# Optimization experiments

Measured on AMD Instinct MI355X. Metric: run time of the kernel, lower is better.

Reference implementation:

```python
import jax, jax.numpy as jnp
import numpy as np
import math

N_HEADS = 16
D_MODEL = 1024
D_K = D_MODEL // N_HEADS
B, T = 16, 512


def setup_inputs() -> dict:
    key = jax.random.key(0)
    ks = jax.random.split(key, 8)
    x = jax.random.normal(ks[0], (B, T, D_MODEL), dtype=jnp.float32)
    mask = jnp.ones((B, 1, T), dtype=bool)
    pos = jax.random.normal(ks[1], (1, 2 * T - 1, D_MODEL), dtype=jnp.float32)
    s = 1.0 / math.sqrt(D_MODEL)
    qvk_w = jax.random.normal(ks[2], (D_MODEL, 3 * D_MODEL), dtype=jnp.float32) * s
    qvk_b = jnp.zeros((3 * D_MODEL,), dtype=jnp.float32)
    pos_w = jax.random.normal(ks[3], (D_MODEL, D_MODEL), dtype=jnp.float32) * s
    # xavier_normal on [1,1,nh,d_k]
    pstd = math.sqrt(2.0 / (N_HEADS + D_K))
    posu = jax.random.normal(ks[4], (1, 1, N_HEADS, D_K), dtype=jnp.float32) * pstd
    posv = jax.random.normal(ks[5], (1, 1, N_HEADS, D_K), dtype=jnp.float32) * pstd
    return {"x": x, "mask": mask, "pos": pos, "qvk_w": qvk_w, "qvk_b": qvk_b,
            "pos_w": pos_w, "posu": posu, "posv": posv}


def _shift(matrix_bd):
    # matrix_bd: [b, nh, t, 2t-1] -> gather relative positions -> [b, nh, t, t]
    b, nh, t, _ = matrix_bd.shape
    r = jnp.arange(t)
    rel_pos = (r[None, :] - r[:, None]) + (t - 1)          # [t, t]
    idx = rel_pos[None, None]                               # [1,1,t,t]
    return jnp.take_along_axis(matrix_bd, jnp.broadcast_to(idx, (b, nh, t, t)), axis=3)


def reference(x, mask, pos, qvk_w, qvk_b, pos_w, posu, posv):
    b, t, d = x.shape
    nh, dk = N_HEADS, D_K
    h = x @ qvk_w + qvk_b                                   # [b, t, 3d]
    q, k, v = jnp.split(h, 3, axis=-1)
    q = q.reshape(b, t, nh, dk)                             # [b, t, nh, dk]
    k = k.reshape(b, t, nh, dk).transpose(0, 2, 1, 3)       # [b, nh, t, dk]
    v = v.reshape(b, t, nh, dk).transpose(0, 2, 1, 3)
    p = (pos @ pos_w).reshape(pos.shape[0], -1, nh, dk).transpose(0, 2, 1, 3)  # [1, nh, 2t-1, dk]
    qu = (q + posu).transpose(0, 2, 1, 3)                   # [b, nh, t, dk]
    qv = (q + posv).transpose(0, 2, 1, 3)
    matrix_ac = jnp.einsum('bhtd,bhsd->bhts', qu, k)        # [b, nh, t, t]
    matrix_bd = jnp.einsum('bhtd,hpd->bhtp', qv, p[0])      # [b, nh, t, 2t-1]
    matrix_bd = _shift(matrix_bd)                           # [b, nh, t, t]
    scores = (matrix_ac + matrix_bd) / math.sqrt(dk)
    m = mask[:, None]                                       # [b, 1, 1, t]
    scores = jnp.where(m, scores, -jnp.inf)
    weights = jax.nn.softmax(scores, axis=-1)
    context = jnp.einsum('bhts,bhsd->bhtd', weights, v)     # [b, nh, t, dk]
    context = context.transpose(0, 2, 1, 3).reshape(b, t, nh * dk)
    # enable_output_proj is falsy (dropout_rate=0.0 passed into that slot) -> no output proj
    return context, weights
```

## Files before the change

### kernel.cpp

```cpp
#include <hip/hip_runtime.h>

typedef _Float16 f16;
typedef _Float16 half8 __attribute__((ext_vector_type(8)));
typedef float floatx4 __attribute__((ext_vector_type(4)));

#define MFMA16(a, b, c) __builtin_amdgcn_mfma_f32_16x16x32_f16(a, b, c, 0, 0, 0)

typedef const __attribute__((address_space(1))) unsigned int* gas_t;
typedef __attribute__((address_space(3))) unsigned int* las_t;
__device__ __forceinline__ void gload16(const void* g, void* l) {
    __builtin_amdgcn_global_load_lds((gas_t)g, (las_t)l, 16, 0, 0);
}


__global__ void k_cvt(const float* __restrict__ in, f16* __restrict__ out, int n4) {
    int i = blockIdx.x * blockDim.x + threadIdx.x;
    if (i >= n4) return;
    float4 v = ((const float4*)in)[i];
    struct alignas(8) H4 { f16 a, b, c, d; };
    H4 o{(f16)v.x, (f16)v.y, (f16)v.z, (f16)v.w};
    ((H4*)out)[i] = o;
}

__global__ void k_cvt_pad(const float* __restrict__ in, f16* __restrict__ out, int n4, int n_in) {
    int i = blockIdx.x * blockDim.x + threadIdx.x;
    if (i >= n4) return;
    struct alignas(8) H4 { f16 a, b, c, d; };
    H4 o;
    if (i * 4 < n_in) {
        float4 v = ((const float4*)in)[i];
        o = H4{(f16)v.x, (f16)v.y, (f16)v.z, (f16)v.w};
    } else {
        o = H4{(f16)0.f, (f16)0.f, (f16)0.f, (f16)0.f};
    }
    ((H4*)out)[i] = o;
}

__global__ void k_transpose(const float* __restrict__ in, f16* __restrict__ out, int R, int C) {
    __shared__ float tile[32][33];
    int c0 = blockIdx.x * 32, r0 = blockIdx.y * 32;
    int tx = threadIdx.x & 31, ty = threadIdx.x >> 5;
#pragma unroll
    for (int i = 0; i < 32; i += 8)
        tile[ty + i][tx] = in[(size_t)(r0 + ty + i) * C + c0 + tx];
    __syncthreads();
#pragma unroll
    for (int i = 0; i < 32; i += 8)
        out[(size_t)(c0 + ty + i) * R + r0 + tx] = (f16)tile[tx][ty + i];
}


__device__ __forceinline__ void gemm_core(const f16* __restrict__ A, const f16* __restrict__ Bt,
                                          int K, int m0, int n0, f16* As, f16* Bs,
                                          floatx4 (&acc)[4][4]) {
    const int tid = threadIdx.x;
    const int lane = tid & 63, wave = tid >> 6;
    const int jj = lane & 15, g = lane >> 4;
    const int wm = (wave >> 1) * 64, wn = (wave & 1) * 64;
    const int gp = g ^ ((jj >> 1) & 3);

#pragma unroll
    for (int mt = 0; mt < 4; mt++)
#pragma unroll
        for (int nt = 0; nt < 4; nt++) acc[mt][nt] = floatx4{0.f, 0.f, 0.f, 0.f};

    const int p0 = tid, p1 = 256 + tid;
    const int r0 = p0 >> 2, k0 = (p0 & 3) ^ ((p0 >> 3) & 3);
    const int r1 = p1 >> 2, k1 = (p1 & 3) ^ ((p1 >> 3) & 3);
    const f16* ga0 = A + (size_t)(m0 + r0) * K + k0 * 8;
    const f16* ga1 = A + (size_t)(m0 + r1) * K + k1 * 8;
    const f16* gb0 = Bt + (size_t)(n0 + r0) * K + k0 * 8;
    const f16* gb1 = Bt + (size_t)(n0 + r1) * K + k1 * 8;
    f16* lA0 = As + (wave * 64) * 8;
    f16* lA1 = As + (256 + wave * 64) * 8;
    f16* lB0 = Bs + (wave * 64) * 8;
    f16* lB1 = Bs + (256 + wave * 64) * 8;

    const int iters = K >> 5;
    for (int kt = 0; kt < iters; ++kt) {
        const int ko = kt * 32;
        gload16(ga0 + ko, lA0);
        gload16(ga1 + ko, lA1);
        gload16(gb0 + ko, lB0);
        gload16(gb1 + ko, lB1);
        __syncthreads();
        half8 af[4], bf[4];
#pragma unroll
        for (int mt = 0; mt < 4; mt++)
            af[mt] = ((const half8*)As)[(wm + mt * 16 + jj) * 4 + gp];
#pragma unroll
        for (int nt = 0; nt < 4; nt++)
            bf[nt] = ((const half8*)Bs)[(wn + nt * 16 + jj) * 4 + gp];
#pragma unroll
        for (int mt = 0; mt < 4; mt++)
#pragma unroll
            for (int nt = 0; nt < 4; nt++)
                acc[mt][nt] = MFMA16(af[mt], bf[nt], acc[mt][nt]);
        __syncthreads();
    }
}

__global__ __launch_bounds__(256) void k_gemm_qkv(const f16* __restrict__ xA, const f16* __restrict__ wT,
                                                  const float* __restrict__ bias,
                                                  const float* __restrict__ pu, const float* __restrict__ pv,
                                                  f16* __restrict__ QU, f16* __restrict__ QV,
                                                  f16* __restrict__ Kb, f16* __restrict__ VT) {
    __shared__ __align__(16) f16 smem[16704];
    f16* As = smem;
    f16* Bs = smem + 4096;
    floatx4 acc[4][4];
    int m0 = blockIdx.y * 128, n0 = blockIdx.x * 128;
    gemm_core(xA, wT, 1024, m0, n0, As, Bs, acc);

    int tid = threadIdx.x;
    int lane = tid & 63, wave = tid >> 6;
    int jj = lane & 15, g = lane >> 4;
    int wm = (wave >> 1) * 64, wn = (wave & 1) * 64;
    int sect = n0 >> 10;

    if (sect == 2) {
        __syncthreads();
        f16* tb = smem;
#pragma unroll
        for (int nt = 0; nt < 4; nt++) {
            int col = wn + nt * 16 + jj;
            float bsv = bias[n0 + col];
#pragma unroll
            for (int mt = 0; mt < 4; mt++)
#pragma unroll
                for (int r = 0; r < 4; r++) {
                    int row = wm + mt * 16 + g * 4 + r;
                    tb[col * 130 + row] = (f16)(acc[mt][nt][r] + bsv);
                }
        }
        __syncthreads();
        int col = tid >> 1, hh = tid & 1;
        int C = n0 + col, head = (C & 1023) >> 6, dk = C & 63;
        int R = m0 + hh * 64, b = R >> 9, tt = R & 511;
        int bh = b * 16 + head;
        f16* dst = VT + ((size_t)bh * 64 + dk) * 512 + tt;
        const f16* srcp = tb + col * 130 + hh * 64;
#pragma unroll
        for (int i = 0; i < 8; i++)
            *(uint4*)(dst + i * 8) = *(const uint4*)(srcp + i * 8);
        return;
    }

#pragma unroll
    for (int nt = 0; nt < 4; nt++) {
        int C = n0 + wn + nt * 16 + jj;
        int cc = C & 1023, head = cc >> 6, dk = cc & 63;
        float bsv = bias[C];
        float uu = pu[cc], vv = pv[cc];
#pragma unroll
        for (int mt = 0; mt < 4; mt++) {
#pragma unroll
            for (int r = 0; r < 4; r++) {
                int R = m0 + wm + mt * 16 + g * 4 + r;
                int b = R >> 9, tt = R & 511;
                int bh = b * 16 + head;
                float val = acc[mt][nt][r] + bsv;
                if (sect == 0) {
                    QU[((size_t)bh * 512 + tt) * 64 + dk] = (f16)(val + uu);
                    QV[((size_t)bh * 512 + tt) * 64 + dk] = (f16)(val + vv);
                } else {
                    Kb[((size_t)bh * 512 + tt) * 64 + dk] = (f16)val;
                }
            }
        }
    }
}

__global__ __launch_bounds__(256) void k_gemm_p(const f16* __restrict__ posA, const f16* __restrict__ pwT,
                                                f16* __restrict__ P) {
    __shared__ __align__(16) f16 As[4096];
    __shared__ __align__(16) f16 Bs[4096];
    floatx4 acc[4][4];
    int m0 = blockIdx.y * 128, n0 = blockIdx.x * 128;
    gemm_core(posA, pwT, 1024, m0, n0, As, Bs, acc);

    int lane = threadIdx.x & 63, wave = threadIdx.x >> 6;
    int jj = lane & 15, g = lane >> 4;
    int wm = (wave >> 1) * 64, wn = (wave & 1) * 64;
#pragma unroll
    for (int nt = 0; nt < 4; nt++) {
        int C = n0 + wn + nt * 16 + jj;
        int head = C >> 6, dk = C & 63;
#pragma unroll
        for (int mt = 0; mt < 4; mt++) {
#pragma unroll
            for (int r = 0; r < 4; r++) {
                int R = m0 + wm + mt * 16 + g * 4 + r;
                float val = (R < 1023) ? acc[mt][nt][r] : 0.0f;
                P[((size_t)head * 1024 + R) * 64 + dk] = (f16)val;
            }
        }
    }
}

__global__ __launch_bounds__(128, 3) void k_attn(const f16* __restrict__ QU, const f16* __restrict__ QV,
                                                 const f16* __restrict__ Kb, const f16* __restrict__ VT,
                                                 const f16* __restrict__ P,
                                                 float* __restrict__ outc, float* __restrict__ outw) {
    __shared__ __align__(16) f16 wbuf[2][16][264];
    __shared__ float redmax[2][16];
    __shared__ float redsum[2][16];
    __shared__ __align__(16) float cbuf[64][20];
    int lane = threadIdx.x & 63;
    int q = threadIdx.x >> 6;
    int bh = blockIdx.x >> 5, rb = blockIdx.x & 31;
    int b = bh >> 4, h = bh & 15;
    int R0 = rb * 16;
    int jj = lane & 15, g = lane >> 4;

    const f16* qub = QU + ((size_t)bh * 512 + R0) * 64;
    const f16* qvb = QV + ((size_t)bh * 512 + R0) * 64;
    const f16* kb = Kb + ((size_t)bh * 512 + q * 256) * 64;
    const f16* vtb = VT + (size_t)bh * 64 * 512;
    const f16* pb = P + (size_t)h * 1024 * 64;

    half8 qu0 = *(const half8*)(qub + jj * 64 + g * 8);
    half8 qu1 = *(const half8*)(qub + jj * 64 + 32 + g * 8);
    half8 qv0 = *(const half8*)(qvb + jj * 64 + g * 8);
    half8 qv1 = *(const half8*)(qvb + jj * 64 + 32 + g * 8);

    floatx4 S[16];
#pragma unroll
    for (int f = 0; f < 16; f++) S[f] = floatx4{0.f, 0.f, 0.f, 0.f};

#pragma unroll
    for (int jt = 0; jt < 16; jt++) {
        half8 b0 = *(const half8*)(kb + (jt * 16 + jj) * 64 + g * 8);
        half8 b1 = *(const half8*)(kb + (jt * 16 + jj) * 64 + 32 + g * 8);
        S[jt] = MFMA16(qu0, b0, S[jt]);
        S[jt] = MFMA16(qu1, b1, S[jt]);
    }

    int U0 = 496 - R0 + q * 256;
    int sl[4];
    bool cond[4];
#pragma unroll
    for (int r = 0; r < 4; r++) {
        int ii = g * 4 + r;
        sl[r] = (lane & 48) | ((jj + 15 - ii) & 15);
        cond[r] = (jj <= ii);
    }
#pragma unroll
    for (int t = 0; t < 17; t++) {
        const f16* prow = pb + (U0 + t * 16 + jj) * 64;
        half8 p0 = *(const half8*)(prow + g * 8);
        half8 p1 = *(const half8*)(prow + 32 + g * 8);
        floatx4 raw = floatx4{0.f, 0.f, 0.f, 0.f};
        raw = MFMA16(qv0, p0, raw);
        raw = MFMA16(qv1, p1, raw);
#pragma unroll
        for (int r = 0; r < 4; r++) {
            float rv = __shfl(raw[r], sl[r], 64);
            float lowv = cond[r] ? rv : 0.0f;
            float hiv = cond[r] ? 0.0f : rv;
            if (t < 16) S[t][r] += lowv;
            if (t > 0) S[t - 1][r] += hiv;
        }
    }

    float mx[4], sm[4], inv[4];
#pragma unroll
    for (int r = 0; r < 4; r++) {
        float m = -1e30f;
#pragma unroll
        for (int f = 0; f < 16; f++) m = fmaxf(m, S[f][r]);
        m = fmaxf(m, __shfl_xor(m, 1, 64));
        m = fmaxf(m, __shfl_xor(m, 2, 64));
        m = fmaxf(m, __shfl_xor(m, 4, 64));
        m = fmaxf(m, __shfl_xor(m, 8, 64));
        mx[r] = m;
        if (jj == 0) redmax[q][g * 4 + r] = m;
    }
    __syncthreads();
#pragma unroll
    for (int r = 0; r < 4; r++) mx[r] = fmaxf(mx[r], redmax[q ^ 1][g * 4 + r]);
#pragma unroll
    for (int f = 0; f < 16; f++)
#pragma unroll
        for (int r = 0; r < 4; r++) S[f][r] = __expf((S[f][r] - mx[r]) * 0.125f);
#pragma unroll
    for (int r = 0; r < 4; r++) {
        float s = 0.f;
#pragma unroll
        for (int f = 0; f < 16; f++) s += S[f][r];
        s += __shfl_xor(s, 1, 64);
        s += __shfl_xor(s, 2, 64);
        s += __shfl_xor(s, 4, 64);
        s += __shfl_xor(s, 8, 64);
        sm[r] = s;
        if (jj == 0) redsum[q][g * 4 + r] = s;
    }
    __syncthreads();
#pragma unroll
    for (int r = 0; r < 4; r++) inv[r] = 1.0f / (sm[r] + redsum[q ^ 1][g * 4 + r]);

    floatx4 ctx[4];
#pragma unroll
    for (int nt = 0; nt < 4; nt++) ctx[nt] = floatx4{0.f, 0.f, 0.f, 0.f};
    float* wrow = outw + ((size_t)bh * 512 + R0) * 512 + q * 256;
#pragma unroll
    for (int f = 0; f < 16; f++) {
#pragma unroll
        for (int r = 0; r < 4; r++) {
            float wv = S[f][r] * inv[r];
            int ii = g * 4 + r;
            __builtin_nontemporal_store(wv, &wrow[(size_t)ii * 512 + f * 16 + jj]);
            wbuf[q][ii][f * 16 + jj] = (f16)wv;
        }
    }
#pragma unroll
    for (int kk = 0; kk < 8; kk++) {
        half8 af = *(const half8*)(&wbuf[q][0][0] + jj * 264 + kk * 32 + g * 8);
#pragma unroll
        for (int nt = 0; nt < 4; nt++) {
            half8 bf = *(const half8*)(vtb + (nt * 16 + jj) * 512 + q * 256 + kk * 32 + g * 8);
            ctx[nt] = MFMA16(af, bf, ctx[nt]);
        }
    }

    if (q == 1) {
#pragma unroll
        for (int nt = 0; nt < 4; nt++)
            *(floatx4*)(&cbuf[lane][nt * 4]) = ctx[nt];
    }
    __syncthreads();
    if (q == 0) {
        float* crow = outc + ((size_t)b * 512 + R0) * 1024 + h * 64;
#pragma unroll
        for (int nt = 0; nt < 4; nt++) {
            floatx4 o = ctx[nt] + *(const floatx4*)(&cbuf[lane][nt * 4]);
#pragma unroll
            for (int r = 0; r < 4; r++)
                __builtin_nontemporal_store(o[r], &crow[(size_t)(g * 4 + r) * 1024 + nt * 16 + jj]);
        }
    }
}


extern "C" void kernel_launch(void* const* d_in, const int* in_sizes, int n_in,
                              void* d_out, int out_size, void* d_ws, size_t ws_size,
                              hipStream_t stream) {
    const float* x = (const float*)d_in[0];
    const float* pos = (const float*)d_in[2];
    const float* qvk_w = (const float*)d_in[3];
    const float* qvk_b = (const float*)d_in[4];
    const float* pos_w = (const float*)d_in[5];
    const float* pu = (const float*)d_in[6];
    const float* pv = (const float*)d_in[7];

    float* outc = (float*)d_out;
    float* outw = outc + (size_t)16 * 512 * 1024;

    char* ws = (char*)d_ws;
    f16* xA = (f16*)(ws);
    f16* wT = (f16*)(ws + 16777216);
    f16* posA = (f16*)(ws + 23068672);
    f16* pwT = (f16*)(ws + 25165824);
    f16* QU = (f16*)(ws + 27262976);
    f16* QV = (f16*)(ws + 44040192);
    f16* Kb = (f16*)(ws + 60817408);
    f16* VT = (f16*)(ws + 77594624);
    f16* Pp = (f16*)(ws + 94371840);

    k_cvt<<<8192, 256, 0, stream>>>(x, xA, 2097152);
    k_cvt_pad<<<1024, 256, 0, stream>>>(pos, posA, 262144, 1047552);
    k_transpose<<<dim3(96, 32), 256, 0, stream>>>(qvk_w, wT, 1024, 3072);
    k_transpose<<<dim3(32, 32), 256, 0, stream>>>(pos_w, pwT, 1024, 1024);

    k_gemm_qkv<<<dim3(24, 64), 256, 0, stream>>>(xA, wT, qvk_b, pu, pv, QU, QV, Kb, VT);
    k_gemm_p<<<dim3(8, 8), 256, 0, stream>>>(posA, pwT, Pp);

    k_attn<<<8192, 128, 0, stream>>>(QU, QV, Kb, VT, Pp, outc, outw);
}
```

Baseline: 612.7 us.

## Stage QKV epilogue through LDS for coalesced stores; raise attention occupancy

The Q/K epilogue of the QKV GEMM now writes the accumulator tile into shared memory and then stores it with coalesced 16-byte writes, replacing scattered 2-byte global stores. Q takes two passes, one for QU and one for QV. The attention kernel reuses the weight buffer for the context reduction to save LDS, raises its launch-bounds occupancy hint from 3 to 4 blocks, and swizzles the block index to change scheduling order. The trade-offs are extra barriers, possible register pressure under the higher occupancy hint, and the removal of the barrier before the V-section transpose (presumably relying on gemm_core's trailing sync).

```diff
diff --git a/kernel.cpp b/kernel.cpp
--- a/kernel.cpp
+++ b/kernel.cpp
@@ -105,7 +105,7 @@
                                                   const float* __restrict__ pu, const float* __restrict__ pv,
                                                   f16* __restrict__ QU, f16* __restrict__ QV,
                                                   f16* __restrict__ Kb, f16* __restrict__ VT) {
-    __shared__ __align__(16) f16 smem[16704];
+    __shared__ __align__(16) f16 smem[16896];
     f16* As = smem;
     f16* Bs = smem + 4096;
     floatx4 acc[4][4];
@@ -119,7 +119,6 @@
     int sect = n0 >> 10;
 
     if (sect == 2) {
-        __syncthreads();
         f16* tb = smem;
 #pragma unroll
         for (int nt = 0; nt < 4; nt++) {
@@ -146,27 +145,34 @@
         return;
     }
 
-#pragma unroll
-    for (int nt = 0; nt < 4; nt++) {
-        int C = n0 + wn + nt * 16 + jj;
-        int cc = C & 1023, head = cc >> 6, dk = cc & 63;
-        float bsv = bias[C];
-        float uu = pu[cc], vv = pv[cc];
-#pragma unroll
-        for (int mt = 0; mt < 4; mt++) {
-#pragma unroll
-            for (int r = 0; r < 4; r++) {
-                int R = m0 + wm + mt * 16 + g * 4 + r;
-                int b = R >> 9, tt = R & 511;
-                int bh = b * 16 + head;
-                float val = acc[mt][nt][r] + bsv;
-                if (sect == 0) {
-                    QU[((size_t)bh * 512 + tt) * 64 + dk] = (f16)(val + uu);
-                    QV[((size_t)bh * 512 + tt) * 64 + dk] = (f16)(val + vv);
-                } else {
-                    Kb[((size_t)bh * 512 + tt) * 64 + dk] = (f16)val;
+    f16* tile = smem;
+    int passes = (sect == 0) ? 2 : 1;
+    for (int p = 0; p < passes; ++p) {
+        if (p) __syncthreads();
+#pragma unroll
+        for (int nt = 0; nt < 4; nt++) {
+            int col = wn + nt * 16 + jj;
+            int cc = (n0 + col) & 1023;
+            float addv = bias[n0 + col] + (sect == 0 ? (p == 0 ? pu[cc] : pv[cc]) : 0.0f);
+#pragma unroll
+            for (int mt = 0; mt < 4; mt++)
+#pragma unroll
+                for (int r = 0; r < 4; r++) {
+                    int row = wm + mt * 16 + g * 4 + r;
+                    tile[row * 132 + col] = (f16)(acc[mt][nt][r] + addv);
                 }
-            }
+        }
+        __syncthreads();
+        f16* dst = (sect == 0) ? (p == 0 ? QU : QV) : Kb;
+#pragma unroll
+        for (int i = 0; i < 8; i++) {
+            int c = i * 256 + tid;
+            int row = c >> 4, ch = c & 15;
+            int R = m0 + row, b = R >> 9, tt = R & 511;
+            int cc = (n0 + ch * 8) & 1023;
+            int head = cc >> 6, dk = cc & 63;
+            *(uint4*)(dst + ((size_t)(b * 16 + head) * 512 + tt) * 64 + dk) =
+                *(const uint4*)(tile + row * 132 + ch * 8);
         }
     }
 }
@@ -198,17 +204,19 @@
     }
 }
 
-__global__ __launch_bounds__(128, 3) void k_attn(const f16* __restrict__ QU, const f16* __restrict__ QV,
+__global__ __launch_bounds__(128, 4) void k_attn(const f16* __restrict__ QU, const f16* __restrict__ QV,
                                                  const f16* __restrict__ Kb, const f16* __restrict__ VT,
                                                  const f16* __restrict__ P,
                                                  float* __restrict__ outc, float* __restrict__ outw) {
     __shared__ __align__(16) f16 wbuf[2][16][264];
     __shared__ float redmax[2][16];
     __shared__ float redsum[2][16];
-    __shared__ __align__(16) float cbuf[64][20];
+    float* cbuf = (float*)wbuf;
     int lane = threadIdx.x & 63;
     int q = threadIdx.x >> 6;
-    int bh = blockIdx.x >> 5, rb = blockIdx.x & 31;
+    int bid = blockIdx.x;
+    int swz = (bid & 7) * 1024 + (bid >> 3);
+    int bh = swz >> 5, rb = swz & 31;
     int b = bh >> 4, h = bh & 15;
     int R0 = rb * 16;
     int jj = lane & 15, g = lane >> 4;
@@ -323,17 +331,18 @@
         }
     }
 
+    __syncthreads();
     if (q == 1) {
 #pragma unroll
         for (int nt = 0; nt < 4; nt++)
-            *(floatx4*)(&cbuf[lane][nt * 4]) = ctx[nt];
+            *(floatx4*)(&cbuf[lane * 20 + nt * 4]) = ctx[nt];
     }
     __syncthreads();
     if (q == 0) {
         float* crow = outc + ((size_t)b * 512 + R0) * 1024 + h * 64;
 #pragma unroll
         for (int nt = 0; nt < 4; nt++) {
-            floatx4 o = ctx[nt] + *(const floatx4*)(&cbuf[lane][nt * 4]);
+            floatx4 o = ctx[nt] + *(const floatx4*)(&cbuf[lane * 20 + nt * 4]);
 #pragma unroll
             for (int r = 0; r < 4; r++)
                 __builtin_nontemporal_store(o[r], &crow[(size_t)(g * 4 + r) * 1024 + nt * 16 + jj]);
```

New measurement: 627.0 us. 2.3% more time.
